# Optimization experiments

Measured on AMD Instinct MI355X. Metric: run time of the kernel, lower is better.

## Reference

```python
import jax, jax.numpy as jnp
import numpy as np

B, CIN, H, W = 16, 128, 56, 56
COUT, KH, KW = 256, 3, 3
STRIDE = (1, 1)
PAD = ((1, 1), (1, 1))


def setup_inputs() -> dict:
    key = jax.random.key(0)
    k1, k2, k3 = jax.random.split(key, 3)
    x = jax.random.normal(k1, (B, CIN, H, W), dtype=jnp.float32)
    weight = jax.random.normal(k2, (COUT, CIN, KH, KW), dtype=jnp.float32) * 0.05
    bias = jax.random.normal(k3, (COUT,), dtype=jnp.float32)
    return {"x": x, "weight": weight, "bias": bias}


def reference(x, weight, bias):
    # Conv2d with zero padding, stride 1 -- identical math to the torch
    # unfold+expand+multiply+triple-sum path.
    dn = jax.lax.conv_dimension_numbers(x.shape, weight.shape, ("NCHW", "OIHW", "NCHW"))
    out = jax.lax.conv_general_dilated(x, weight, STRIDE, PAD, dimension_numbers=dn)
    out = out + bias[None, :, None, None]

    # Sparsity of the elementwise product patches * weight.
    # count_nonzero(x_patch * w) over all (b,hw,ww,co,ci,kh,kw) factorizes as
    # sum over windows of conv(1[x!=0], 1[w!=0]) -- same count without
    # materializing the [B,Hw,Ww,Co,Ci,kh,kw] tensor the torch code builds.
    co, ci, kh, kw = weight.shape
    hw, ww = out.shape[2], out.shape[3]
    num_elements = x.shape[0] * hw * ww * co * ci * kh * kw
    nz_map = jax.lax.conv_general_dilated(
        (x != 0).astype(jnp.float32),
        (weight != 0).astype(jnp.float32),
        STRIDE, PAD, dimension_numbers=dn)
    num_nonzero = jnp.sum(nz_map)
    layer_sparsity = (jnp.float32(num_elements) - num_nonzero) / jnp.float32(num_elements)
    return out, layer_sparsity
```

## Files before the change

### kernel.cpp

```cpp
#include <hip/hip_runtime.h>
#include <hip/hip_bf16.h>

typedef __attribute__((ext_vector_type(8))) short bf16x8;
typedef __attribute__((ext_vector_type(8))) unsigned short ushort8;
typedef __attribute__((ext_vector_type(4))) unsigned short ushort4v;
typedef __attribute__((ext_vector_type(4))) float f32x4;
typedef __attribute__((ext_vector_type(4))) unsigned int uint4v;

#define CIN_  128
#define BATCH 16
#define SP_   3136
#define CO_   256
#define NTOT  50176

#define XP_BYTES   13778944
#define WT_BYTES   589824
#define WS_NEEDED  14447104

__device__ __forceinline__ unsigned short f2bf(float f) {
    unsigned int u = __float_as_uint(f);
    u = (u + 0x7fffu + ((u >> 16) & 1u)) >> 16;
    return (unsigned short)u;
}

__device__ __forceinline__ void gl_lds16(const unsigned short* g, unsigned short* l) {
    __builtin_amdgcn_global_load_lds(
        (const __attribute__((address_space(1))) unsigned int*)g,
        (__attribute__((address_space(3))) unsigned int*)l, 16, 0, 0);
}

__global__ __launch_bounds__(256) void k_aux(
    const float* __restrict__ x, const float* __restrict__ w,
    unsigned short* __restrict__ Wt, unsigned short* __restrict__ xp,
    float* __restrict__ Wcnt, float* __restrict__ part)
{
    __shared__ float T[64][65];
    __shared__ float red9[4][9];
    const int blk = blockIdx.x;
    const int tid = threadIdx.x;

    if (blk < 288) {
        int base = (blk * 256 + tid) * 4;
        float4 v = *(const float4*)(w + base);
        #pragma unroll
        for (int j = 0; j < 4; ++j) {
            int e = base + j;
            int co = e / 1152;
            int r  = e - co * 1152;
            int ci = r / 9;
            int koff = r - ci * 9;
            Wt[(koff * 256 + co) * 128 + ci] = f2bf(((const float*)&v)[j]);
        }
    } else if (blk < 576) {
        int lane = tid & 63;
        int j = (blk - 288) * 4 + (tid >> 6);
        float c = 0.f;
        for (int co = lane; co < 256; co += 64)
            c += (w[(size_t)co * 1152 + j] != 0.0f) ? 1.f : 0.f;
        #pragma unroll
        for (int s = 32; s > 0; s >>= 1) c += __shfl_down(c, s, 64);
        if (lane == 0) Wcnt[j] = c;
    } else if (blk < 2624) {
        int bc = blk - 576;
        int ci = bc & 127;
        int b  = bc >> 7;
        const float* xpk = x + (size_t)bc * SP_;
        float cnt[9];
        #pragma unroll
        for (int k = 0; k < 9; ++k) cnt[k] = 0.f;
        for (int e = tid; e < SP_; e += 256) {
            float v = xpk[e];
            if (v != 0.f) {
                int h = e / 56, w_ = e - h * 56;
                float r0 = (h <= 54) ? 1.f : 0.f;
                float r2 = (h >= 1) ? 1.f : 0.f;
                float c0 = (w_ <= 54) ? 1.f : 0.f;
                float c2 = (w_ >= 1) ? 1.f : 0.f;
                cnt[0] += r0 * c0; cnt[1] += r0; cnt[2] += r0 * c2;
                cnt[3] += c0;      cnt[4] += 1.f; cnt[5] += c2;
                cnt[6] += r2 * c0; cnt[7] += r2; cnt[8] += r2 * c2;
            }
        }
        #pragma unroll
        for (int k = 0; k < 9; ++k) {
            #pragma unroll
            for (int s = 32; s > 0; s >>= 1) cnt[k] += __shfl_down(cnt[k], s, 64);
        }
        if ((tid & 63) == 0) {
            #pragma unroll
            for (int k = 0; k < 9; ++k) red9[tid >> 6][k] = cnt[k];
        }
        __syncthreads();
        if (tid < 9) {
            float s = red9[0][tid] + red9[1][tid] + red9[2][tid] + red9[3][tid];
            part[(ci * 9 + tid) * 16 + b] = s;
        }
    } else if (blk < 4192) {
        int i = blk - 2624;
        int sp0 = (i % 49) * 64;
        int rest = i / 49;
        int ci0 = (rest & 1) * 64;
        int b = rest >> 1;
        const float* xb = x + ((size_t)(b * 128 + ci0)) * SP_ + sp0;
        #pragma unroll
        for (int r = 0; r < 16; ++r) {
            const int ci_l = (tid >> 6) * 16 + r;
            const int sp_l = tid & 63;
            T[sp_l][ci_l] = xb[(size_t)ci_l * SP_ + sp_l];
        }
        __syncthreads();
        #pragma unroll
        for (int r = 0; r < 4; ++r) {
            const int sp_l = (tid >> 4) * 4 + r;
            const int cc   = (tid & 15) * 4;
            const int sp = sp0 + sp_l;
            const int oh = sp / 56, ow = sp - oh * 56;
            ushort4v v;
            #pragma unroll
            for (int j = 0; j < 4; ++j) v[j] = f2bf(T[sp_l][cc + j]);
            *(ushort4v*)&xp[(((size_t)b * 58 + oh + 1) * 58 + (ow + 1)) * 128 + ci0 + cc] = v;
        }
    } else {
        int b = blk - 4192;
        if (tid < 228) {
            int oh, ow;
            if (tid < 58)       { oh = 0;            ow = tid; }
            else if (tid < 116) { oh = 57;           ow = tid - 58; }
            else if (tid < 172) { oh = tid - 116 + 1; ow = 0; }
            else                { oh = tid - 172 + 1; ow = 57; }
            unsigned short* p = xp + (((size_t)b * 58 + oh) * 58 + ow) * 128;
            ushort8 z = {};
            #pragma unroll
            for (int j = 0; j < 16; ++j) *(ushort8*)(p + j * 8) = z;
        }
    }
}

__global__ __launch_bounds__(512, 2) void k_conv8(
    const unsigned short* __restrict__ xp, const unsigned short* __restrict__ Wt,
    const float* __restrict__ bias, float* __restrict__ out,
    const float* __restrict__ Wcnt, const float* __restrict__ part)
{
    __shared__ __attribute__((aligned(16))) unsigned short Albs[2 * 16384];
    __shared__ __attribute__((aligned(16))) unsigned short Blbs[2 * 16384];

    const int tid  = threadIdx.x;

    if (blockIdx.x == 196) {
        double* red = (double*)Albs;
        double s = 0.0;
        for (int j = tid; j < 1152; j += 512) {
            const float4* p4 = (const float4*)(part + (size_t)j * 16);
            float4 a = p4[0], b = p4[1], c = p4[2], d = p4[3];
            float xs = (a.x + a.y + a.z + a.w) + (b.x + b.y + b.z + b.w)
                     + (c.x + c.y + c.z + c.w) + (d.x + d.y + d.z + d.w);
            s += (double)Wcnt[j] * (double)xs;
        }
        red[tid] = s; __syncthreads();
        for (int k = 256; k > 0; k >>= 1) {
            if (tid < k) red[tid] += red[tid + k];
            __syncthreads();
        }
        if (tid == 0) {
            const double ne = 14797504512.0;
            out[12845056] = (float)((ne - red[0]) / ne);
        }
        return;
    }

    const int lane = tid & 63;
    const int l15  = lane & 15;
    const int w    = tid >> 6;
    const int wm   = w >> 2;
    const int wn   = w & 3;
    const int n0   = blockIdx.x * 256;

    int xoffA[2], woffB[2];
    #pragma unroll
    for (int j = 0; j < 2; ++j) {
        int g   = j * 512 + tid;
        int row = g >> 2;
        int c   = (g & 3) ^ ((row >> 1) & 3);
        int n   = n0 + row;
        int b   = n / SP_;
        int sp  = n - b * SP_;
        int oh  = sp / 56, ow = sp - oh * 56;
        xoffA[j] = ((b * 58 + oh + 1) * 58 + (ow + 1)) * 128 + c * 8;
        woffB[j] = row * 128 + c * 8;
    }

    auto stageA = [&](int nb, int xsh, int s) {
        #pragma unroll
        for (int j = 0; j < 2; ++j)
            gl_lds16(xp + xsh + s * 32 + xoffA[j],
                     &Albs[nb + s * 8192 + (j * 512 + tid) * 8]);
    };
    auto stageB = [&](int nb, int wsh, int s) {
        #pragma unroll
        for (int j = 0; j < 2; ++j)
            gl_lds16(Wt + wsh + s * 32 + woffB[j],
                     &Blbs[nb + s * 8192 + (j * 512 + tid) * 8]);
    };

    f32x4 acc[8][4] = {};
    const int cl = lane >> 4;

#define LDA_(bo, S, R) \
    (*(const bf16x8*)&Albs[(bo) + (S) * 8192 + ((R) + l15) * 32 + \
        ((cl ^ ((((R) + l15) >> 1) & 3)) * 8)])
#define LDB_(bo, S, R) \
    (*(const bf16x8*)&Blbs[(bo) + (S) * 8192 + ((R) + l15) * 32 + \
        ((cl ^ ((((R) + l15) >> 1) & 3)) * 8)])

#define PHASE(BO, S, DO_STAGE, NB, XSH, WSH, VMN)                          \
    {                                                                      \
        if (DO_STAGE) { stageA(NB, XSH, S); stageB(NB, WSH, S); }          \
        asm volatile("s_waitcnt vmcnt(" VMN ")" ::: "memory");             \
        __builtin_amdgcn_s_barrier();                                      \
        bf16x8 b_[4], a_[8];                                               \
        _Pragma("unroll")                                                  \
        for (int nn = 0; nn < 4; ++nn) b_[nn] = LDB_(BO, S, wn * 64 + nn * 16);\
        _Pragma("unroll")                                                  \
        for (int m = 0; m < 8; ++m) a_[m] = LDA_(BO, S, wm * 128 + m * 16);\
        __builtin_amdgcn_s_setprio(1);                                     \
        _Pragma("unroll")                                                  \
        for (int m = 0; m < 8; ++m)                                        \
            _Pragma("unroll")                                              \
            for (int nn = 0; nn < 4; ++nn)                                 \
                acc[m][nn] = __builtin_amdgcn_mfma_f32_16x16x32_bf16(      \
                    a_[m], b_[nn], acc[m][nn], 0, 0, 0);                   \
        __builtin_amdgcn_s_setprio(0);                                     \
    }

    {
        const int xsh0 = (-59) * 128;
        stageA(0, xsh0, 0); stageB(0, 0, 0);
        stageA(0, xsh0, 1); stageB(0, 0, 1);
    }

    for (int kt = 0; kt < 17; ++kt) {
        const int bo = (kt & 1) << 14;
        const int nb = 16384 - bo;
        const int kn = kt + 1;
        const int koffn = kn >> 1;
        const int kdn = koffn / 3;
        const int xshn = ((kdn - 1) * 58 + (koffn - kdn * 3 - 1)) * 128 + (kn & 1) * 64;
        const int wshn = koffn * 32768 + (kn & 1) * 64;
        PHASE(bo, 0, true, nb, xshn, wshn, "8");
        PHASE(bo, 1, true, nb, xshn, wshn, "8");
    }
    PHASE(16384, 0, false, 0, 0, 0, "4");
    PHASE(16384, 1, false, 0, 0, 0, "0");

#undef PHASE
#undef LDA_
#undef LDB_

    #pragma unroll
    for (int m = 0; m < 8; ++m) {
        int n  = n0 + wm * 128 + m * 16 + (lane >> 4) * 4;
        int b  = n / SP_;
        int sp = n - b * SP_;
        #pragma unroll
        for (int nn = 0; nn < 4; ++nn) {
            int co = wn * 64 + nn * 16 + l15;
            f32x4 v = acc[m][nn] + bias[co];
            *(f32x4*)&out[((size_t)(b * CO_ + co)) * SP_ + sp] = v;
        }
    }
}

__global__ void k_wt(const float* __restrict__ w, unsigned short* __restrict__ Wt) {
    int e = blockIdx.x * 256 + threadIdx.x;
    float v = w[e];
    int co = e / 1152;
    int r  = e - co * 1152;
    int ci = r / 9;
    int koff = r - ci * 9;
    Wt[(koff * 256 + co) * 128 + ci] = f2bf(v);
}

__global__ void k_wcnt(const float* __restrict__ w, float* __restrict__ Wcnt) {
    int j = blockIdx.x;
    int lane = threadIdx.x;
    float c = 0.f;
    for (int co = lane; co < 256; co += 64)
        c += (w[(size_t)co * 1152 + j] != 0.0f) ? 1.f : 0.f;
    #pragma unroll
    for (int s = 32; s > 0; s >>= 1) c += __shfl_down(c, s, 64);
    if (lane == 0) Wcnt[j] = c;
}

__global__ void k_xcnt(const float* __restrict__ x, float* __restrict__ Xcnt) {
    int blk = blockIdx.x;
    int ci = blk & 127;
    const float* xpk = x + (size_t)blk * SP_;
    int tid = threadIdx.x;
    float cnt[9];
    #pragma unroll
    for (int k = 0; k < 9; ++k) cnt[k] = 0.f;
    for (int e = tid; e < SP_; e += 256) {
        float v = xpk[e];
        if (v != 0.f) {
            int h = e / 56, w_ = e - h * 56;
            float r0 = (h <= 54) ? 1.f : 0.f;
            float r2 = (h >= 1) ? 1.f : 0.f;
            float c0 = (w_ <= 54) ? 1.f : 0.f;
            float c2 = (w_ >= 1) ? 1.f : 0.f;
            cnt[0] += r0 * c0; cnt[1] += r0; cnt[2] += r0 * c2;
            cnt[3] += c0;      cnt[4] += 1.f; cnt[5] += c2;
            cnt[6] += r2 * c0; cnt[7] += r2; cnt[8] += r2 * c2;
        }
    }
    #pragma unroll
    for (int k = 0; k < 9; ++k) {
        #pragma unroll
        for (int s = 32; s > 0; s >>= 1) cnt[k] += __shfl_down(cnt[k], s, 64);
    }
    if ((tid & 63) == 0) {
        #pragma unroll
        for (int k = 0; k < 9; ++k)
            atomicAdd(&Xcnt[ci * 9 + k], cnt[k]);
    }
}

__global__ void k_spars_f(const float* __restrict__ Wcnt, const float* __restrict__ Xcnt,
                          float* __restrict__ out_scalar) {
    __shared__ double red[256];
    int t = threadIdx.x;
    double s = 0.0;
    for (int j = t; j < 1152; j += 256)
        s += (double)Wcnt[j] * (double)Xcnt[j];
    red[t] = s; __syncthreads();
    for (int k = 128; k > 0; k >>= 1) {
        if (t < k) red[t] += red[t + k];
        __syncthreads();
    }
    if (t == 0) {
        const double ne = 14797504512.0;
        out_scalar[0] = (float)((ne - red[0]) / ne);
    }
}

__global__ __launch_bounds__(256) void k_conv(
    const float* __restrict__ x, const unsigned short* __restrict__ Wt,
    const float* __restrict__ bias, float* __restrict__ out)
{
    __shared__ __attribute__((aligned(16))) unsigned short AldsF[64][40];
    __shared__ __attribute__((aligned(16))) unsigned short BldsF[64][40];

    const int tid  = threadIdx.x;
    const int lane = tid & 63;
    const int wid  = tid >> 6;
    const int wm   = wid >> 1, wn = wid & 1;

    const int n0  = blockIdx.x * 64;
    const int b   = blockIdx.x / 49;
    const int sp0 = n0 - b * SP_;
    const int co0 = blockIdx.y * 64;

    const int a_co = tid >> 2;
    const int a_ci = (tid & 3) * 8;
    const int b_n  = tid & 63;
    const int b_k0 = (tid >> 6) * 8;

    const int sp = sp0 + b_n;
    const int oh = sp / 56, ow = sp - oh * 56;

    f32x4 acc[2][2] = {};
    const float* xb_base = x + (size_t)b * CIN_ * SP_;

    for (int koff = 0; koff < 9; ++koff) {
        const int dh = koff / 3 - 1, dw = koff - (koff / 3) * 3 - 1;
        const int ih = oh + dh, iw = ow + dw;
        const bool valid = ((unsigned)ih < 56u) && ((unsigned)iw < 56u);
        const float* xb = xb_base + sp + dh * 56 + dw;
        const unsigned short* wp = Wt + ((size_t)(koff * 256 + co0 + a_co)) * 128 + a_ci;

        for (int ci0 = 0; ci0 < 128; ci0 += 32) {
            uint4v av = *(const uint4v*)(wp + ci0);
            *(uint4v*)&AldsF[a_co][a_ci] = av;
            ushort8 bv;
            #pragma unroll
            for (int j = 0; j < 8; ++j) {
                int ci = ci0 + b_k0 + j;
                float v = 0.f;
                if (valid) v = xb[(size_t)ci * SP_];
                bv[j] = f2bf(v);
            }
            *(ushort8*)&BldsF[b_n][b_k0] = bv;
            __syncthreads();

            const int row = lane & 15;
            const int kq  = (lane >> 4) * 8;
            bf16x8 a0 = *(const bf16x8*)&AldsF[wm * 32 + row][kq];
            bf16x8 a1 = *(const bf16x8*)&AldsF[wm * 32 + 16 + row][kq];
            bf16x8 bb0 = *(const bf16x8*)&BldsF[wn * 32 + row][kq];
            bf16x8 bb1 = *(const bf16x8*)&BldsF[wn * 32 + 16 + row][kq];
            acc[0][0] = __builtin_amdgcn_mfma_f32_16x16x32_bf16(a0, bb0, acc[0][0], 0, 0, 0);
            acc[0][1] = __builtin_amdgcn_mfma_f32_16x16x32_bf16(a0, bb1, acc[0][1], 0, 0, 0);
            acc[1][0] = __builtin_amdgcn_mfma_f32_16x16x32_bf16(a1, bb0, acc[1][0], 0, 0, 0);
            acc[1][1] = __builtin_amdgcn_mfma_f32_16x16x32_bf16(a1, bb1, acc[1][1], 0, 0, 0);
            __syncthreads();
        }
    }

    const int col = lane & 15;
    const int rb  = (lane >> 4) * 4;
    #pragma unroll
    for (int f = 0; f < 2; ++f) {
        #pragma unroll
        for (int g = 0; g < 2; ++g) {
            int spc = sp0 + wn * 32 + g * 16 + col;
            #pragma unroll
            for (int r = 0; r < 4; ++r) {
                int co = co0 + wm * 32 + f * 16 + rb + r;
                out[((size_t)(b * CO_ + co)) * SP_ + spc] = acc[f][g][r] + bias[co];
            }
        }
    }
}

extern "C" void kernel_launch(void* const* d_in, const int* in_sizes, int n_in,
                              void* d_out, int out_size, void* d_ws, size_t ws_size,
                              hipStream_t stream) {
    const float* x    = (const float*)d_in[0];
    const float* w    = (const float*)d_in[1];
    const float* bias = (const float*)d_in[2];
    float* out = (float*)d_out;

    if (ws_size >= (size_t)WS_NEEDED) {
        unsigned short* xp = (unsigned short*)d_ws;
        unsigned short* Wt = (unsigned short*)((char*)d_ws + XP_BYTES);
        float* Wcnt = (float*)((char*)d_ws + XP_BYTES + WT_BYTES);
        float* part = Wcnt + 1152;

        hipLaunchKernelGGL(k_aux,   dim3(4208),   dim3(256), 0, stream,
                           x, w, Wt, xp, Wcnt, part);
        hipLaunchKernelGGL(k_conv8, dim3(197),    dim3(512), 0, stream,
                           xp, Wt, bias, out, Wcnt, part);
    } else {
        unsigned short* Wt = (unsigned short*)d_ws;
        float* Wcnt = (float*)((char*)d_ws + WT_BYTES);
        float* Xcnt = Wcnt + 1152;

        hipMemsetAsync((void*)Xcnt, 0, 1152 * sizeof(float), stream);
        hipLaunchKernelGGL(k_wt,      dim3(1152),    dim3(256), 0, stream, w, Wt);
        hipLaunchKernelGGL(k_wcnt,    dim3(1152),    dim3(64),  0, stream, w, Wcnt);
        hipLaunchKernelGGL(k_xcnt,    dim3(2048),    dim3(256), 0, stream, x, Xcnt);
        hipLaunchKernelGGL(k_conv,    dim3(784, 4),  dim3(256), 0, stream, x, Wt, bias, out);
        hipLaunchKernelGGL(k_spars_f, dim3(1),       dim3(256), 0, stream, Wcnt, Xcnt,
                           out + 12845056);
    }
}
```

Measured before the change: 60.28 us.

## Restructure aux prep: 64x64 transpose tiles with fused per-tap nonzero counts

Adds a new aux kernel that transposes x to padded NHWC bf16 in 64-channel by 64-position tiles (fewer, larger blocks than before). Each block also computes per-channel, per-kernel-tap nonzero counts with boundary masks and writes 576 partials, so the sparsity count can be formed directly as a dot product with the weight nonzero counts. The conv kernel's reduction block gains a mode that sums about 900K partials against Wcnt. The aim is to cut aux launch and block overhead, at the cost of a much larger final reduction done by a single block and a larger workspace requirement.

```diff
diff --git a/kernel.cpp b/kernel.cpp
--- a/kernel.cpp
+++ b/kernel.cpp
@@ -13,9 +13,10 @@
 #define CO_   256
 #define NTOT  50176
 
-#define XP_BYTES   13778944
-#define WT_BYTES   589824
-#define WS_NEEDED  14447104
+#define XP_BYTES    13778944
+#define WT_BYTES    589824
+#define WS_NEEDED   14447104
+#define WS2_NEEDED  17986048
 
 __device__ __forceinline__ unsigned short f2bf(float f) {
     unsigned int u = __float_as_uint(f);
@@ -27,6 +28,112 @@
     __builtin_amdgcn_global_load_lds(
         (const __attribute__((address_space(1))) unsigned int*)g,
         (__attribute__((address_space(3))) unsigned int*)l, 16, 0, 0);
+}
+
+__global__ __launch_bounds__(256) void k_aux2(
+    const float* __restrict__ x, const float* __restrict__ w,
+    unsigned short* __restrict__ Wt, unsigned short* __restrict__ xp,
+    float* __restrict__ Wcnt, float* __restrict__ part2)
+{
+    __shared__ float T[64][65];
+    __shared__ float R2[4][64][9];
+    const int blk = blockIdx.x;
+    const int tid = threadIdx.x;
+
+    if (blk < 288) {
+        int base = (blk * 256 + tid) * 4;
+        float4 v = *(const float4*)(w + base);
+        #pragma unroll
+        for (int j = 0; j < 4; ++j) {
+            int e = base + j;
+            int co = e / 1152;
+            int r  = e - co * 1152;
+            int ci = r / 9;
+            int koff = r - ci * 9;
+            Wt[(koff * 256 + co) * 128 + ci] = f2bf(((const float*)&v)[j]);
+        }
+    } else if (blk < 576) {
+        int lane = tid & 63;
+        int j = (blk - 288) * 4 + (tid >> 6);
+        float c = 0.f;
+        for (int co = lane; co < 256; co += 64)
+            c += (w[(size_t)co * 1152 + j] != 0.0f) ? 1.f : 0.f;
+        #pragma unroll
+        for (int s = 32; s > 0; s >>= 1) c += __shfl_down(c, s, 64);
+        if (lane == 0) Wcnt[j] = c;
+    } else if (blk < 2144) {
+        int xi = blk - 576;
+        int chunk = xi % 49;
+        int rest  = xi / 49;
+        int half  = rest & 1;
+        int b     = rest >> 1;
+        int sp0   = chunk * 64;
+        int ci0   = half * 64;
+        const float* xb = x + ((size_t)(b * 128 + ci0)) * SP_ + sp0;
+        #pragma unroll
+        for (int r = 0; r < 16; ++r) {
+            const int ci_l = (tid >> 6) * 16 + r;
+            const int sp_l = tid & 63;
+            T[sp_l][ci_l] = xb[(size_t)ci_l * SP_ + sp_l];
+        }
+        __syncthreads();
+        #pragma unroll
+        for (int r = 0; r < 4; ++r) {
+            const int sp_l = (tid >> 4) * 4 + r;
+            const int cc   = (tid & 15) * 4;
+            const int sp = sp0 + sp_l;
+            const int oh = sp / 56, ow = sp - oh * 56;
+            ushort4v v;
+            #pragma unroll
+            for (int j = 0; j < 4; ++j) v[j] = f2bf(T[sp_l][cc + j]);
+            *(ushort4v*)&xp[(((size_t)b * 58 + oh + 1) * 58 + (ow + 1)) * 128 + ci0 + cc] = v;
+        }
+        {
+            const int ci_l = tid & 63;
+            const int q    = tid >> 6;
+            float cnt[9];
+            #pragma unroll
+            for (int k = 0; k < 9; ++k) cnt[k] = 0.f;
+            #pragma unroll
+            for (int s = 0; s < 16; ++s) {
+                const int sp_l = q * 16 + s;
+                float v = T[sp_l][ci_l];
+                if (v != 0.f) {
+                    int sp = sp0 + sp_l;
+                    int h = sp / 56, w_ = sp - h * 56;
+                    float r0 = (h <= 54) ? 1.f : 0.f;
+                    float r2 = (h >= 1) ? 1.f : 0.f;
+                    float c0 = (w_ <= 54) ? 1.f : 0.f;
+                    float c2 = (w_ >= 1) ? 1.f : 0.f;
+                    cnt[0] += r0 * c0; cnt[1] += r0; cnt[2] += r0 * c2;
+                    cnt[3] += c0;      cnt[4] += 1.f; cnt[5] += c2;
+                    cnt[6] += r2 * c0; cnt[7] += r2; cnt[8] += r2 * c2;
+                }
+            }
+            #pragma unroll
+            for (int k = 0; k < 9; ++k) R2[q][ci_l][k] = cnt[k];
+        }
+        __syncthreads();
+        for (int idx = tid; idx < 576; idx += 256) {
+            int ci = idx / 9;
+            int k  = idx - ci * 9;
+            float s4 = R2[0][ci][k] + R2[1][ci][k] + R2[2][ci][k] + R2[3][ci][k];
+            part2[(size_t)xi * 576 + idx] = s4;
+        }
+    } else {
+        int b = blk - 2144;
+        if (tid < 228) {
+            int oh, ow;
+            if (tid < 58)       { oh = 0;            ow = tid; }
+            else if (tid < 116) { oh = 57;           ow = tid - 58; }
+            else if (tid < 172) { oh = tid - 116 + 1; ow = 0; }
+            else                { oh = tid - 172 + 1; ow = 57; }
+            unsigned short* p = xp + (((size_t)b * 58 + oh) * 58 + ow) * 128;
+            ushort8 z = {};
+            #pragma unroll
+            for (int j = 0; j < 16; ++j) *(ushort8*)(p + j * 8) = z;
+        }
+    }
 }
 
 __global__ __launch_bounds__(256) void k_aux(
@@ -139,7 +246,7 @@
 __global__ __launch_bounds__(512, 2) void k_conv8(
     const unsigned short* __restrict__ xp, const unsigned short* __restrict__ Wt,
     const float* __restrict__ bias, float* __restrict__ out,
-    const float* __restrict__ Wcnt, const float* __restrict__ part)
+    const float* __restrict__ Wcnt, const float* __restrict__ part, int pmode)
 {
     __shared__ __attribute__((aligned(16))) unsigned short Albs[2 * 16384];
     __shared__ __attribute__((aligned(16))) unsigned short Blbs[2 * 16384];
@@ -149,12 +256,23 @@
     if (blockIdx.x == 196) {
         double* red = (double*)Albs;
         double s = 0.0;
-        for (int j = tid; j < 1152; j += 512) {
-            const float4* p4 = (const float4*)(part + (size_t)j * 16);
-            float4 a = p4[0], b = p4[1], c = p4[2], d = p4[3];
-            float xs = (a.x + a.y + a.z + a.w) + (b.x + b.y + b.z + b.w)
-                     + (c.x + c.y + c.z + c.w) + (d.x + d.y + d.z + d.w);
-            s += (double)Wcnt[j] * (double)xs;
+        if (pmode == 1) {
+            for (int f = tid * 4; f < 1568 * 576; f += 2048) {
+                int bi   = f / 576;
+                int e    = f - bi * 576;
+                int half = (bi / 49) & 1;
+                const float* wc = Wcnt + half * 576 + e;
+                float4 v = *(const float4*)(part + f);
+                s += (double)(wc[0] * v.x + wc[1] * v.y + wc[2] * v.z + wc[3] * v.w);
+            }
+        } else {
+            for (int j = tid; j < 1152; j += 512) {
+                const float4* p4 = (const float4*)(part + (size_t)j * 16);
+                float4 a = p4[0], b = p4[1], c = p4[2], d = p4[3];
+                float xs = (a.x + a.y + a.z + a.w) + (b.x + b.y + b.z + b.w)
+                         + (c.x + c.y + c.z + c.w) + (d.x + d.y + d.z + d.w);
+                s += (double)Wcnt[j] * (double)xs;
+            }
         }
         red[tid] = s; __syncthreads();
         for (int k = 256; k > 0; k >>= 1) {
@@ -429,7 +547,17 @@
     const float* bias = (const float*)d_in[2];
     float* out = (float*)d_out;
 
-    if (ws_size >= (size_t)WS_NEEDED) {
+    if (ws_size >= (size_t)WS2_NEEDED) {
+        unsigned short* xp = (unsigned short*)d_ws;
+        unsigned short* Wt = (unsigned short*)((char*)d_ws + XP_BYTES);
+        float* Wcnt  = (float*)((char*)d_ws + XP_BYTES + WT_BYTES);
+        float* part2 = Wcnt + 1152;
+
+        hipLaunchKernelGGL(k_aux2,  dim3(2160),   dim3(256), 0, stream,
+                           x, w, Wt, xp, Wcnt, part2);
+        hipLaunchKernelGGL(k_conv8, dim3(197),    dim3(512), 0, stream,
+                           xp, Wt, bias, out, Wcnt, part2, 1);
+    } else if (ws_size >= (size_t)WS_NEEDED) {
         unsigned short* xp = (unsigned short*)d_ws;
         unsigned short* Wt = (unsigned short*)((char*)d_ws + XP_BYTES);
         float* Wcnt = (float*)((char*)d_ws + XP_BYTES + WT_BYTES);
@@ -438,7 +566,7 @@
         hipLaunchKernelGGL(k_aux,   dim3(4208),   dim3(256), 0, stream,
                            x, w, Wt, xp, Wcnt, part);
         hipLaunchKernelGGL(k_conv8, dim3(197),    dim3(512), 0, stream,
-                           xp, Wt, bias, out, Wcnt, part);
+                           xp, Wt, bias, out, Wcnt, part, 0);
     } else {
         unsigned short* Wt = (unsigned short*)d_ws;
         float* Wcnt = (float*)((char*)d_ws + WT_BYTES);
```

After: 185.0 us. 207% more time.
